# Performance work log

Hardware: AMD Instinct MI355X
Metric: run time of the kernel (lower is better)

The kernel has to match this reference:

```python
import jax, jax.numpy as jnp
import numpy as np

B, L, H = 2, 2048, 2048
NH, D = 16, 128          # num_heads, head_dim
MLP = 4 * H              # mlp_hidden_dim = int(hidden_size * mlp_ratio)


def setup_inputs() -> dict:
    key = jax.random.key(0)
    ks = jax.random.split(key, 8)
    x = jax.random.normal(ks[0], (B, L, H), jnp.float32)
    vec = jax.random.normal(ks[1], (B, H), jnp.float32)
    pe = jax.random.normal(ks[2], (B, 1, L, D // 2, 2, 2), jnp.float32)
    # Modulation(dim, is_double=False): Linear(H, 3H)
    mod_w = 0.02 * jax.random.normal(ks[3], (3 * H, H), jnp.float32)
    mod_b = jnp.zeros((3 * H,), jnp.float32)
    # linear1: Linear(H, 3H + MLP)
    lin1_w = 0.02 * jax.random.normal(ks[4], (3 * H + MLP, H), jnp.float32)
    lin1_b = jnp.zeros((3 * H + MLP,), jnp.float32)
    # linear2: Linear(H + MLP, H)
    lin2_w = 0.02 * jax.random.normal(ks[5], (H, H + MLP), jnp.float32)
    lin2_b = jnp.zeros((H,), jnp.float32)
    # QKNorm: RMSNorm scales over head_dim
    q_scale = jnp.ones((D,), jnp.float32)
    k_scale = jnp.ones((D,), jnp.float32)
    return dict(x=x, vec=vec, pe=pe, mod_w=mod_w, mod_b=mod_b,
                lin1_w=lin1_w, lin1_b=lin1_b, lin2_w=lin2_w, lin2_b=lin2_b,
                q_scale=q_scale, k_scale=k_scale)


def _layernorm(x, eps=1e-6):
    mu = jnp.mean(x, axis=-1, keepdims=True)
    var = jnp.mean((x - mu) ** 2, axis=-1, keepdims=True)
    return (x - mu) * jax.lax.rsqrt(var + eps)


def _rmsnorm(x, scale, eps=1e-6):
    return x * jax.lax.rsqrt(jnp.mean(x * x, axis=-1, keepdims=True) + eps) * scale


def _apply_rope(t, pe):
    # t: [B, NH, L, D]; pe: [B, 1, L, D//2, 2, 2]
    t_ = t.reshape(*t.shape[:-1], D // 2, 1, 2)
    out = pe[..., 0] * t_[..., 0] + pe[..., 1] * t_[..., 1]  # [B, NH, L, D//2, 2]
    return out.reshape(*t.shape)


def reference(x, vec, pe, mod_w, mod_b, lin1_w, lin1_b, lin2_w, lin2_b, q_scale, k_scale):
    # Modulation: silu -> linear -> (shift, scale, gate), each [B, 1, H]
    mod = jax.nn.silu(vec) @ mod_w.T + mod_b
    shift, scale, gate = jnp.split(mod[:, None, :], 3, axis=-1)

    x_mod = (1.0 + scale) * _layernorm(x) + shift

    h = x_mod @ lin1_w.T + lin1_b            # [B, L, 3H + MLP]
    qkv, mlp = h[..., :3 * H], h[..., 3 * H:]

    # 'B L (K H D) -> K B H L D'
    qkv = qkv.reshape(B, L, 3, NH, D).transpose(2, 0, 3, 1, 4)
    q, k, v = qkv[0], qkv[1], qkv[2]

    q = _rmsnorm(q, q_scale)
    k = _rmsnorm(k, k_scale)

    q = _apply_rope(q, pe)
    k = _apply_rope(k, pe)

    # SDPA with default scale 1/sqrt(D)
    logits = jnp.einsum('bhqd,bhkd->bhqk', q, k) / jnp.sqrt(jnp.float32(D))
    probs = jax.nn.softmax(logits, axis=-1)
    attn = jnp.einsum('bhqk,bhkd->bhqd', probs, v)          # [B, NH, L, D]
    attn = attn.transpose(0, 2, 1, 3).reshape(B, L, H)      # 'B H L D -> B L (H D)'

    mlp_act = jax.nn.gelu(mlp, approximate=True)
    out = jnp.concatenate([attn, mlp_act], axis=-1) @ lin2_w.T + lin2_b
    return x + gate * out
```

## Files before the change

kernel.cpp:

```cpp
#include <hip/hip_runtime.h>

#define LSEQ 2048
#define HDIM 2048
#define NHEAD 16
#define DHEAD 128
#define N1 14336
#define NC 10240

typedef unsigned short u16;
typedef __attribute__((ext_vector_type(8))) short short8;
typedef __attribute__((ext_vector_type(4))) float f32x4;

#define ASYNC16(g, l) __builtin_amdgcn_global_load_lds( \
    (__attribute__((address_space(1))) void*)(g),        \
    (__attribute__((address_space(3))) void*)(l), 16, 0, 0)

__device__ __forceinline__ u16 f2bf(float f) {
  unsigned u = __builtin_bit_cast(unsigned, f);
  u += 0x7fffu + ((u >> 16) & 1u);
  return (u16)(u >> 16);
}
__device__ __forceinline__ float bf2f(u16 v) {
  unsigned u = ((unsigned)v) << 16;
  return __builtin_bit_cast(float, u);
}
__device__ __forceinline__ float silu_f(float x) { return x / (1.f + __expf(-x)); }
__device__ __forceinline__ float gelu_f(float x) {
  float u = 0.7978845608028654f * (x + 0.044715f * x * x * x);
  float e = __expf(2.f * u);
  float th = 1.f - 2.f / (e + 1.f);
  return 0.5f * x * (1.f + th);
}

__global__ __launch_bounds__(256) void k_mod(const float* __restrict__ vec,
                                             const float* __restrict__ mod_w,
                                             const float* __restrict__ mod_b,
                                             float* __restrict__ modv) {
  int j = blockIdx.x, t = threadIdx.x;
  const float4* wr = (const float4*)(mod_w + (size_t)j * HDIM);
  const float4* vv = (const float4*)vec;
  float s0 = 0.f, s1 = 0.f;
#pragma unroll
  for (int i = 0; i < 2; i++) {
    int idx = t + i * 256;
    float4 w = wr[idx];
    float4 a = vv[idx];
    float4 c = vv[idx + 512];
    s0 += w.x*silu_f(a.x) + w.y*silu_f(a.y) + w.z*silu_f(a.z) + w.w*silu_f(a.w);
    s1 += w.x*silu_f(c.x) + w.y*silu_f(c.y) + w.z*silu_f(c.z) + w.w*silu_f(c.w);
  }
  int lane = t & 63, wid = t >> 6;
#pragma unroll
  for (int o = 32; o; o >>= 1) { s0 += __shfl_down(s0, o, 64); s1 += __shfl_down(s1, o, 64); }
  __shared__ float red[8];
  if (!lane) { red[wid] = s0; red[4 + wid] = s1; }
  __syncthreads();
  if (!t) {
    float b_ = mod_b[j];
    modv[j] = red[0]+red[1]+red[2]+red[3] + b_;
    modv[3*HDIM + j] = red[4]+red[5]+red[6]+red[7] + b_;
  }
}

__global__ __launch_bounds__(256) void k_ln(const float* __restrict__ x,
                                            const float* __restrict__ modv,
                                            u16* __restrict__ xmod) {
  int row = blockIdx.x, t = threadIdx.x;
  int b = row >> 11;
  const float4* xr = (const float4*)(x + (size_t)row * HDIM);
  float4 v0 = xr[t], v1 = xr[t + 256];
  float sum = v0.x+v0.y+v0.z+v0.w + v1.x+v1.y+v1.z+v1.w;
  float sq  = v0.x*v0.x+v0.y*v0.y+v0.z*v0.z+v0.w*v0.w
            + v1.x*v1.x+v1.y*v1.y+v1.z*v1.z+v1.w*v1.w;
  int lane = t & 63, wid = t >> 6;
#pragma unroll
  for (int o = 32; o; o >>= 1) { sum += __shfl_down(sum, o, 64); sq += __shfl_down(sq, o, 64); }
  __shared__ float red[8];
  if (!lane) { red[wid] = sum; red[4+wid] = sq; }
  __syncthreads();
  sum = red[0]+red[1]+red[2]+red[3];
  sq  = red[4]+red[5]+red[6]+red[7];
  float mu = sum * (1.f/HDIM);
  float rstd = rsqrtf(sq * (1.f/HDIM) - mu*mu + 1e-6f);
  const float* mb = modv + b * (3*HDIM);
  u16* orow = xmod + (size_t)row * HDIM;
  float vv[8] = {v0.x,v0.y,v0.z,v0.w,v1.x,v1.y,v1.z,v1.w};
#pragma unroll
  for (int half = 0; half < 2; half++) {
    int h0 = (t + half*256) * 4;
    ushort4 o4;
    float e0 = (1.f + mb[HDIM + h0+0]) * ((vv[half*4+0]-mu)*rstd) + mb[h0+0];
    float e1 = (1.f + mb[HDIM + h0+1]) * ((vv[half*4+1]-mu)*rstd) + mb[h0+1];
    float e2 = (1.f + mb[HDIM + h0+2]) * ((vv[half*4+2]-mu)*rstd) + mb[h0+2];
    float e3 = (1.f + mb[HDIM + h0+3]) * ((vv[half*4+3]-mu)*rstd) + mb[h0+3];
    o4.x = f2bf(e0); o4.y = f2bf(e1); o4.z = f2bf(e2); o4.w = f2bf(e3);
    *(ushort4*)(orow + h0) = o4;
  }
}

__global__ __launch_bounds__(256) void k_cvt(const float4* __restrict__ src,
                                             ushort4* __restrict__ dst, int n4) {
  int i = blockIdx.x * 256 + threadIdx.x;
  int stride = gridDim.x * 256;
  for (; i < n4; i += stride) {
    float4 v = src[i];
    ushort4 o;
    o.x = f2bf(v.x); o.y = f2bf(v.y); o.z = f2bf(v.z); o.w = f2bf(v.w);
    dst[i] = o;
  }
}

__global__ __launch_bounds__(256, 2) void k_gemm1(const u16* __restrict__ A,
                                                  const u16* __restrict__ Bw,
                                                  const float* __restrict__ bias,
                                                  u16* __restrict__ qkv,
                                                  u16* __restrict__ cat) {
  const int K = HDIM;
  const int NB = N1 / 128;
  int bid = blockIdx.x;
  int bm = bid / NB, bn = bid % NB;
  int t = threadIdx.x, wave = t >> 6, lane = t & 63;
  int wm = wave >> 1, wn = wave & 1;
  __shared__ u16 S[128 * 136];
  u16* As = S;
  u16* Bs = S + 4096;
  const f32x4 fzero = {0.f, 0.f, 0.f, 0.f};
  f32x4 acc[4][4];
#pragma unroll
  for (int i = 0; i < 4; i++)
#pragma unroll
    for (int j2 = 0; j2 < 4; j2++) acc[i][j2] = fzero;
  const u16* Ab = A + (size_t)bm * 128 * K;
  const u16* Bb = Bw + (size_t)bn * 128 * K;
  int r4 = lane >> 2, c4 = lane & 3;
  int fm = lane & 15, fk = (lane >> 4) * 8, fq = lane >> 4;
  for (int k0 = 0; k0 < K; k0 += 32) {
#pragma unroll
    for (int i = 0; i < 2; i++) {
      int row = wave*32 + i*16;
      ASYNC16(Ab + (size_t)(row + r4)*K + k0 + c4*8, &As[row*32]);
      ASYNC16(Bb + (size_t)(row + r4)*K + k0 + c4*8, &Bs[row*32]);
    }
    __syncthreads();
    short8 af[4], bfr[4];
#pragma unroll
    for (int mt = 0; mt < 4; mt++)
      af[mt] = *(const short8*)&As[(wm*64 + mt*16 + fm)*32 + fk];
#pragma unroll
    for (int nt = 0; nt < 4; nt++)
      bfr[nt] = *(const short8*)&Bs[(wn*64 + nt*16 + fm)*32 + fk];
#pragma unroll
    for (int mt = 0; mt < 4; mt++)
#pragma unroll
      for (int nt = 0; nt < 4; nt++)
        acc[mt][nt] = __builtin_amdgcn_mfma_f32_16x16x32_bf16(af[mt], bfr[nt], acc[mt][nt], 0, 0, 0);
    __syncthreads();
  }
  bool ismlp = (bn >= 48);
#pragma unroll
  for (int nt = 0; nt < 4; nt++) {
    int col_l = wn*64 + nt*16 + fm;
    float bv = bias[bn*128 + col_l];
#pragma unroll
    for (int mt = 0; mt < 4; mt++) {
#pragma unroll
      for (int rr = 0; rr < 4; rr++) {
        int row_l = wm*64 + mt*16 + fq*4 + rr;
        float v = acc[mt][nt][rr] + bv;
        if (ismlp) v = gelu_f(v);
        S[row_l*136 + col_l] = f2bf(v);
      }
    }
  }
  __syncthreads();
  int c = (t & 15) * 8;
  int rq = t >> 4;
#pragma unroll
  for (int p = 0; p < 8; p++) {
    int r_l = p*16 + rq;
    short8 v = *(const short8*)&S[r_l*136 + c];
    int row_g = bm*128 + r_l;
    if (!ismlp)
      *(short8*)(qkv + (size_t)row_g*(3*HDIM) + bn*128 + c) = v;
    else
      *(short8*)(cat + (size_t)row_g*NC + HDIM + (bn-48)*128 + c) = v;
  }
}

__global__ __launch_bounds__(256, 2) void k_gemm2(const u16* __restrict__ A,
                                                  const u16* __restrict__ Bw,
                                                  const float* __restrict__ bias,
                                                  const float* __restrict__ xres,
                                                  const float* __restrict__ modv,
                                                  float* __restrict__ out) {
  const int K = NC;
  const int NB = HDIM / 128;
  int bid = blockIdx.x;
  int bm = bid / NB, bn = bid % NB;
  int t = threadIdx.x, wave = t >> 6, lane = t & 63;
  int wm = wave >> 1, wn = wave & 1;
  __shared__ u16 As[128 * 32];
  __shared__ u16 Bs[128 * 32];
  const f32x4 fzero = {0.f, 0.f, 0.f, 0.f};
  f32x4 acc[4][4];
#pragma unroll
  for (int i = 0; i < 4; i++)
#pragma unroll
    for (int j2 = 0; j2 < 4; j2++) acc[i][j2] = fzero;
  const u16* Ab = A + (size_t)bm * 128 * K;
  const u16* Bb = Bw + (size_t)bn * 128 * K;
  int r4 = lane >> 2, c4 = lane & 3;
  int fm = lane & 15, fk = (lane >> 4) * 8;
  for (int k0 = 0; k0 < K; k0 += 32) {
#pragma unroll
    for (int i = 0; i < 2; i++) {
      int row = wave*32 + i*16;
      ASYNC16(Ab + (size_t)(row + r4)*K + k0 + c4*8, &As[row*32]);
      ASYNC16(Bb + (size_t)(row + r4)*K + k0 + c4*8, &Bs[row*32]);
    }
    __syncthreads();
    short8 af[4], bfr[4];
#pragma unroll
    for (int mt = 0; mt < 4; mt++)
      af[mt] = *(const short8*)&As[(wm*64 + mt*16 + fm)*32 + fk];
#pragma unroll
    for (int nt = 0; nt < 4; nt++)
      bfr[nt] = *(const short8*)&Bs[(wn*64 + nt*16 + fm)*32 + fk];
#pragma unroll
    for (int mt = 0; mt < 4; mt++)
#pragma unroll
      for (int nt = 0; nt < 4; nt++)
        acc[mt][nt] = __builtin_amdgcn_mfma_f32_16x16x32_bf16(af[mt], bfr[nt], acc[mt][nt], 0, 0, 0);
    __syncthreads();
  }
  int rbase = bm*128 + wm*64;
  int cbase = bn*128 + wn*64;
  int b = (bm*128) >> 11;
#pragma unroll
  for (int nt = 0; nt < 4; nt++) {
    int col = cbase + nt*16 + fm;
    float bv = bias[col];
    float g = modv[b*(3*HDIM) + 2*HDIM + col];
#pragma unroll
    for (int mt = 0; mt < 4; mt++) {
#pragma unroll
      for (int rr = 0; rr < 4; rr++) {
        int row = rbase + mt*16 + (lane>>4)*4 + rr;
        size_t idx = (size_t)row*HDIM + col;
        out[idx] = xres[idx] + g * (acc[mt][nt][rr] + bv);
      }
    }
  }
}

__global__ __launch_bounds__(256) void k_qk(const u16* __restrict__ qkv,
                                            const float* __restrict__ pe,
                                            const float* __restrict__ q_scale,
                                            const float* __restrict__ k_scale,
                                            u16* __restrict__ Q, u16* __restrict__ Ko) {
  int bid = blockIdx.x;
  int l = bid & (LSEQ-1);
  int b = bid >> 11;
  int t = threadIdx.x;
  int h = t >> 4;
  int dc = (t & 15) * 8;
  const u16* base = qkv + (size_t)bid * (3*HDIM);
  short8 q8 = *(const short8*)(base + h*DHEAD + dc);
  short8 k8 = *(const short8*)(base + HDIM + h*DHEAD + dc);
  float qf[8], kf[8];
  float sq = 0.f, sk = 0.f;
#pragma unroll
  for (int i = 0; i < 8; i++) {
    qf[i] = bf2f((u16)q8[i]); kf[i] = bf2f((u16)k8[i]);
    sq += qf[i]*qf[i]; sk += kf[i]*kf[i];
  }
#pragma unroll
  for (int m = 1; m < 16; m <<= 1) { sq += __shfl_xor(sq, m, 64); sk += __shfl_xor(sk, m, 64); }
  float rq = rsqrtf(sq * (1.f/DHEAD) + 1e-6f);
  float rk = rsqrtf(sk * (1.f/DHEAD) + 1e-6f);
  float4 qs0 = *(const float4*)(q_scale + dc), qs1 = *(const float4*)(q_scale + dc + 4);
  float4 ks0 = *(const float4*)(k_scale + dc), ks1 = *(const float4*)(k_scale + dc + 4);
  float qsc[8] = {qs0.x,qs0.y,qs0.z,qs0.w,qs1.x,qs1.y,qs1.z,qs1.w};
  float ksc[8] = {ks0.x,ks0.y,ks0.z,ks0.w,ks1.x,ks1.y,ks1.z,ks1.w};
  float qn[8], kn[8];
#pragma unroll
  for (int i = 0; i < 8; i++) { qn[i] = qf[i]*rq*qsc[i]; kn[i] = kf[i]*rk*ksc[i]; }
  const float4* pe4 = (const float4*)pe + ((size_t)bid*64 + (dc >> 1));
  short8 qo, ko;
#pragma unroll
  for (int pi = 0; pi < 4; pi++) {
    float4 pp = pe4[pi];
    float q0 = pp.x*qn[2*pi] + pp.y*qn[2*pi+1];
    float q1 = pp.z*qn[2*pi] + pp.w*qn[2*pi+1];
    float k0 = pp.x*kn[2*pi] + pp.y*kn[2*pi+1];
    float k1 = pp.z*kn[2*pi] + pp.w*kn[2*pi+1];
    qo[2*pi] = (short)f2bf(q0); qo[2*pi+1] = (short)f2bf(q1);
    ko[2*pi] = (short)f2bf(k0); ko[2*pi+1] = (short)f2bf(k1);
  }
  size_t oidx = (((size_t)(b*NHEAD + h))*LSEQ + l)*DHEAD + dc;
  *(short8*)(Q + oidx) = qo;
  *(short8*)(Ko + oidx) = ko;
}

__global__ __launch_bounds__(256) void k_vt(const u16* __restrict__ qkv, u16* __restrict__ Vt) {
  int bid = blockIdx.x;
  int lt = bid & 31, h = (bid >> 5) & 15, b = bid >> 9;
  __shared__ u16 tile[64][132];
  int t = threadIdx.x;
#pragma unroll
  for (int it = 0; it < 8; it++) {
    int idx = it*1024 + t*4;
    int li = idx >> 7, di = idx & 127;
    const u16* src = qkv + ((size_t)(b*LSEQ + lt*64 + li))*(3*HDIM) + 2*HDIM + h*DHEAD + di;
    ushort4 v = *(const ushort4*)src;
    *(ushort4*)&tile[li][di] = v;
  }
  __syncthreads();
  u16* dst = Vt + ((size_t)(b*NHEAD + h))*DHEAD*LSEQ + lt*64;
#pragma unroll
  for (int it = 0; it < 32; it++) {
    int idx = it*256 + t;
    int lo = idx & 63, dd = idx >> 6;
    dst[(size_t)dd*LSEQ + lo] = tile[lo][dd];
  }
}

#define ATT_SCALE 0.08838834764831845f
__global__ __launch_bounds__(256, 2) void k_attn(const u16* __restrict__ Q,
                                                 const u16* __restrict__ Kc,
                                                 const u16* __restrict__ Vt,
                                                 u16* __restrict__ cat) {
  __shared__ u16 Ks[2*64*128];
  __shared__ u16 Vs[2*128*64];
  __shared__ u16 Ps[64*88];
  int bid = blockIdx.x;
  int bh = bid & 31, qt = bid >> 5;
  int h = bh & 15, b = bh >> 4;
  int t = threadIdx.x, wave = t >> 6, lane = t & 63;
  int fm = lane & 15, fq = lane >> 4;
  int r8 = lane >> 3, c8 = lane & 7;
  const u16* Qg = Q  + (((size_t)(b*NHEAD + h))*LSEQ + qt*64) * DHEAD;
  const u16* Kg = Kc + ((size_t)(b*NHEAD + h))*LSEQ * DHEAD;
  const u16* Vg = Vt + ((size_t)(b*NHEAD + h))*DHEAD*LSEQ;
  short8 aq[4];
#pragma unroll
  for (int ks = 0; ks < 4; ks++)
    aq[ks] = *(const short8*)(Qg + (size_t)(wave*16 + fm)*DHEAD + ks*32 + fq*8);
#pragma unroll
  for (int i = 0; i < 4; i++) {
    int row = wave*16 + i*4;
    ASYNC16(Kg + (size_t)(row + fq)*DHEAD + fm*8, &Ks[row*DHEAD]);
    int vrow = wave*32 + i*8;
    ASYNC16(Vg + (size_t)(vrow + r8)*LSEQ + c8*8, &Vs[vrow*64]);
  }
  const f32x4 fzero = {0.f, 0.f, 0.f, 0.f};
  f32x4 o[8];
#pragma unroll
  for (int i = 0; i < 8; i++) o[i] = fzero;
  float m_i[4], l_i[4];
#pragma unroll
  for (int r = 0; r < 4; r++) { m_i[r] = -1e30f; l_i[r] = 0.f; }
  for (int kt = 0; kt < 32; kt++) {
    int cur = kt & 1;
    __syncthreads();
    if (kt < 31) {
      int off = (cur ^ 1) * 8192;
      const u16* Kt_ = Kg + (size_t)(kt+1)*64*DHEAD;
      const u16* Vt_ = Vg + (kt+1)*64;
#pragma unroll
      for (int i = 0; i < 4; i++) {
        int row = wave*16 + i*4;
        ASYNC16(Kt_ + (size_t)(row + fq)*DHEAD + fm*8, &Ks[off + row*DHEAD]);
        int vrow = wave*32 + i*8;
        ASYNC16(Vt_ + (size_t)(vrow + r8)*LSEQ + c8*8, &Vs[off + vrow*64]);
      }
    }
    const u16* Kb = &Ks[cur*8192];
    const u16* Vb = &Vs[cur*8192];
    f32x4 s[4];
#pragma unroll
    for (int nt = 0; nt < 4; nt++) s[nt] = fzero;
#pragma unroll
    for (int ks = 0; ks < 4; ks++) {
#pragma unroll
      for (int nt = 0; nt < 4; nt++) {
        short8 bk = *(const short8*)&Kb[(nt*16 + fm)*DHEAD + ks*32 + fq*8];
        s[nt] = __builtin_amdgcn_mfma_f32_16x16x32_bf16(aq[ks], bk, s[nt], 0, 0, 0);
      }
    }
    float rowm[4];
#pragma unroll
    for (int r = 0; r < 4; r++)
      rowm[r] = fmaxf(fmaxf(s[0][r], s[1][r]), fmaxf(s[2][r], s[3][r])) * ATT_SCALE;
#pragma unroll
    for (int r = 0; r < 4; r++) {
#pragma unroll
      for (int o2 = 8; o2 >= 1; o2 >>= 1)
        rowm[r] = fmaxf(rowm[r], __shfl_xor(rowm[r], o2, 64));
    }
    float alpha[4];
#pragma unroll
    for (int r = 0; r < 4; r++) {
      float mnew = fmaxf(m_i[r], rowm[r]);
      alpha[r] = __expf(m_i[r] - mnew);
      m_i[r] = mnew;
    }
    float rs[4] = {0.f, 0.f, 0.f, 0.f};
#pragma unroll
    for (int nt = 0; nt < 4; nt++)
#pragma unroll
      for (int r = 0; r < 4; r++) {
        float p = __expf(s[nt][r] * ATT_SCALE - m_i[r]);
        s[nt][r] = p;
        rs[r] += p;
      }
#pragma unroll
    for (int r = 0; r < 4; r++) {
#pragma unroll
      for (int o2 = 8; o2 >= 1; o2 >>= 1) rs[r] += __shfl_xor(rs[r], o2, 64);
      l_i[r] = l_i[r] * alpha[r] + rs[r];
    }
#pragma unroll
    for (int i = 0; i < 8; i++)
#pragma unroll
      for (int r = 0; r < 4; r++) o[i][r] *= alpha[r];
#pragma unroll
    for (int nt = 0; nt < 4; nt++)
#pragma unroll
      for (int r = 0; r < 4; r++)
        Ps[(wave*16 + fq*4 + r)*88 + nt*16 + fm] = f2bf(s[nt][r]);
    asm volatile("s_waitcnt lgkmcnt(0)" ::: "memory");
#pragma unroll
    for (int ks2 = 0; ks2 < 2; ks2++) {
      short8 ap = *(const short8*)&Ps[(wave*16 + fm)*88 + ks2*32 + fq*8];
#pragma unroll
      for (int nt = 0; nt < 8; nt++) {
        short8 bv = *(const short8*)&Vb[(nt*16 + fm)*64 + ks2*32 + fq*8];
        o[nt] = __builtin_amdgcn_mfma_f32_16x16x32_bf16(ap, bv, o[nt], 0, 0, 0);
      }
    }
  }
#pragma unroll
  for (int nt = 0; nt < 8; nt++) {
#pragma unroll
    for (int r = 0; r < 4; r++) {
      int l = qt*64 + wave*16 + fq*4 + r;
      int d = nt*16 + fm;
      float v = o[nt][r] / l_i[r];
      cat[((size_t)(b*LSEQ + l))*NC + h*DHEAD + d] = f2bf(v);
    }
  }
}

extern "C" void kernel_launch(void* const* d_in, const int* in_sizes, int n_in,
                              void* d_out, int out_size, void* d_ws, size_t ws_size,
                              hipStream_t stream) {
  const float* x       = (const float*)d_in[0];
  const float* vec     = (const float*)d_in[1];
  const float* pe      = (const float*)d_in[2];
  const float* mod_w   = (const float*)d_in[3];
  const float* mod_b   = (const float*)d_in[4];
  const float* lin1_w  = (const float*)d_in[5];
  const float* lin1_b  = (const float*)d_in[6];
  const float* lin2_w  = (const float*)d_in[7];
  const float* lin2_b  = (const float*)d_in[8];
  const float* q_scale = (const float*)d_in[9];
  const float* k_scale = (const float*)d_in[10];
  char* ws = (char*)d_ws;

  float* modv = (float*)(ws + 0);
  u16* xmod  = (u16*)(ws + 65536ULL);
  u16* qkv   = (u16*)(ws + 16842752ULL);
  u16* cat   = (u16*)(ws + 67174400ULL);
  u16* w2    = (u16*)(ws + 151060480ULL);
  u16* w1    = (u16*)(ws + 193003520ULL);
  u16* Qb    = (u16*)(ws + 193003520ULL);
  u16* Kb    = (u16*)(ws + 209780736ULL);
  u16* Vtb   = (u16*)(ws + 226557952ULL);

  k_mod<<<dim3(3*HDIM), dim3(256), 0, stream>>>(vec, mod_w, mod_b, modv);
  k_cvt<<<dim3(4096), dim3(256), 0, stream>>>((const float4*)lin1_w, (ushort4*)w1, (N1*HDIM)/4);
  k_cvt<<<dim3(4096), dim3(256), 0, stream>>>((const float4*)lin2_w, (ushort4*)w2, (HDIM*NC)/4);
  k_ln<<<dim3(4096), dim3(256), 0, stream>>>(x, modv, xmod);
  k_gemm1<<<dim3(32*112), dim3(256), 0, stream>>>(xmod, w1, lin1_b, qkv, cat);
  k_qk<<<dim3(4096), dim3(256), 0, stream>>>(qkv, pe, q_scale, k_scale, Qb, Kb);
  k_vt<<<dim3(1024), dim3(256), 0, stream>>>(qkv, Vtb);
  k_attn<<<dim3(1024), dim3(256), 0, stream>>>(Qb, Kb, Vtb, cat);
  k_gemm2<<<dim3(32*16), dim3(256), 0, stream>>>(cat, w2, lin2_b, x, modv, (float*)d_out);
}
```

Baseline: 1.185 ms.

## Double K-step in GEMMs, drop online-max softmax, reorder blocks and workspace

Both GEMMs now load 64-wide K slices per barrier pair instead of 32, halving synchronisation count, and block indices are remapped so M tiles vary fastest for weight reuse in cache. Attention drops the running max and rescaling, relying on QK-normalised logits being bounded, and uses exp2 with a folded scale plus truncating bf16 conversion for P. The lin2 weight conversion is moved later and placed over the dead qkv region to shrink workspace. The risks are overflow if q/k scales grow, and slightly lower precision from truncation.

Result: faster. 1.012 ms (-14.6%).

```diff
diff --git a/kernel.cpp b/kernel.cpp
--- a/kernel.cpp
+++ b/kernel.cpp
@@ -19,6 +19,9 @@
   unsigned u = __builtin_bit_cast(unsigned, f);
   u += 0x7fffu + ((u >> 16) & 1u);
   return (u16)(u >> 16);
+}
+__device__ __forceinline__ u16 f2bf_trunc(float f) {
+  return (u16)(__builtin_bit_cast(unsigned, f) >> 16);
 }
 __device__ __forceinline__ float bf2f(u16 v) {
   unsigned u = ((unsigned)v) << 16;
@@ -116,14 +119,15 @@
                                                   u16* __restrict__ qkv,
                                                   u16* __restrict__ cat) {
   const int K = HDIM;
-  const int NB = N1 / 128;
   int bid = blockIdx.x;
-  int bm = bid / NB, bn = bid % NB;
+  int bm = bid & 31, bn = bid >> 5;
   int t = threadIdx.x, wave = t >> 6, lane = t & 63;
   int wm = wave >> 1, wn = wave & 1;
   __shared__ u16 S[128 * 136];
-  u16* As = S;
-  u16* Bs = S + 4096;
+  u16* As0 = S;
+  u16* As1 = S + 4096;
+  u16* Bs0 = S + 8192;
+  u16* Bs1 = S + 12288;
   const f32x4 fzero = {0.f, 0.f, 0.f, 0.f};
   f32x4 acc[4][4];
 #pragma unroll
@@ -134,26 +138,35 @@
   const u16* Bb = Bw + (size_t)bn * 128 * K;
   int r4 = lane >> 2, c4 = lane & 3;
   int fm = lane & 15, fk = (lane >> 4) * 8, fq = lane >> 4;
-  for (int k0 = 0; k0 < K; k0 += 32) {
+  for (int k0 = 0; k0 < K; k0 += 64) {
 #pragma unroll
     for (int i = 0; i < 2; i++) {
       int row = wave*32 + i*16;
-      ASYNC16(Ab + (size_t)(row + r4)*K + k0 + c4*8, &As[row*32]);
-      ASYNC16(Bb + (size_t)(row + r4)*K + k0 + c4*8, &Bs[row*32]);
+      const u16* ar = Ab + (size_t)(row + r4)*K + k0 + c4*8;
+      const u16* br = Bb + (size_t)(row + r4)*K + k0 + c4*8;
+      ASYNC16(ar,      &As0[row*32]);
+      ASYNC16(ar + 32, &As1[row*32]);
+      ASYNC16(br,      &Bs0[row*32]);
+      ASYNC16(br + 32, &Bs1[row*32]);
     }
     __syncthreads();
-    short8 af[4], bfr[4];
-#pragma unroll
-    for (int mt = 0; mt < 4; mt++)
-      af[mt] = *(const short8*)&As[(wm*64 + mt*16 + fm)*32 + fk];
-#pragma unroll
-    for (int nt = 0; nt < 4; nt++)
-      bfr[nt] = *(const short8*)&Bs[(wn*64 + nt*16 + fm)*32 + fk];
-#pragma unroll
-    for (int mt = 0; mt < 4; mt++)
+#pragma unroll
+    for (int p = 0; p < 2; p++) {
+      const u16* Ap = p ? As1 : As0;
+      const u16* Bp = p ? Bs1 : Bs0;
+      short8 af[4], bfr[4];
+#pragma unroll
+      for (int mt = 0; mt < 4; mt++)
+        af[mt] = *(const short8*)&Ap[(wm*64 + mt*16 + fm)*32 + fk];
 #pragma unroll
       for (int nt = 0; nt < 4; nt++)
-        acc[mt][nt] = __builtin_amdgcn_mfma_f32_16x16x32_bf16(af[mt], bfr[nt], acc[mt][nt], 0, 0, 0);
+        bfr[nt] = *(const short8*)&Bp[(wn*64 + nt*16 + fm)*32 + fk];
+#pragma unroll
+      for (int mt = 0; mt < 4; mt++)
+#pragma unroll
+        for (int nt = 0; nt < 4; nt++)
+          acc[mt][nt] = __builtin_amdgcn_mfma_f32_16x16x32_bf16(af[mt], bfr[nt], acc[mt][nt], 0, 0, 0);
+    }
     __syncthreads();
   }
   bool ismlp = (bn >= 48);
@@ -194,13 +207,12 @@
                                                   const float* __restrict__ modv,
                                                   float* __restrict__ out) {
   const int K = NC;
-  const int NB = HDIM / 128;
   int bid = blockIdx.x;
-  int bm = bid / NB, bn = bid % NB;
+  int bm = bid & 31, bn = bid >> 5;
   int t = threadIdx.x, wave = t >> 6, lane = t & 63;
   int wm = wave >> 1, wn = wave & 1;
-  __shared__ u16 As[128 * 32];
-  __shared__ u16 Bs[128 * 32];
+  __shared__ u16 As[2*128*32];
+  __shared__ u16 Bs[2*128*32];
   const f32x4 fzero = {0.f, 0.f, 0.f, 0.f};
   f32x4 acc[4][4];
 #pragma unroll
@@ -211,26 +223,35 @@
   const u16* Bb = Bw + (size_t)bn * 128 * K;
   int r4 = lane >> 2, c4 = lane & 3;
   int fm = lane & 15, fk = (lane >> 4) * 8;
-  for (int k0 = 0; k0 < K; k0 += 32) {
+  for (int k0 = 0; k0 < K; k0 += 64) {
 #pragma unroll
     for (int i = 0; i < 2; i++) {
       int row = wave*32 + i*16;
-      ASYNC16(Ab + (size_t)(row + r4)*K + k0 + c4*8, &As[row*32]);
-      ASYNC16(Bb + (size_t)(row + r4)*K + k0 + c4*8, &Bs[row*32]);
+      const u16* ar = Ab + (size_t)(row + r4)*K + k0 + c4*8;
+      const u16* br = Bb + (size_t)(row + r4)*K + k0 + c4*8;
+      ASYNC16(ar,      &As[row*32]);
+      ASYNC16(ar + 32, &As[4096 + row*32]);
+      ASYNC16(br,      &Bs[row*32]);
+      ASYNC16(br + 32, &Bs[4096 + row*32]);
     }
     __syncthreads();
-    short8 af[4], bfr[4];
-#pragma unroll
-    for (int mt = 0; mt < 4; mt++)
-      af[mt] = *(const short8*)&As[(wm*64 + mt*16 + fm)*32 + fk];
-#pragma unroll
-    for (int nt = 0; nt < 4; nt++)
-      bfr[nt] = *(const short8*)&Bs[(wn*64 + nt*16 + fm)*32 + fk];
-#pragma unroll
-    for (int mt = 0; mt < 4; mt++)
+#pragma unroll
+    for (int p = 0; p < 2; p++) {
+      const u16* Ap = &As[p*4096];
+      const u16* Bp = &Bs[p*4096];
+      short8 af[4], bfr[4];
+#pragma unroll
+      for (int mt = 0; mt < 4; mt++)
+        af[mt] = *(const short8*)&Ap[(wm*64 + mt*16 + fm)*32 + fk];
 #pragma unroll
       for (int nt = 0; nt < 4; nt++)
-        acc[mt][nt] = __builtin_amdgcn_mfma_f32_16x16x32_bf16(af[mt], bfr[nt], acc[mt][nt], 0, 0, 0);
+        bfr[nt] = *(const short8*)&Bp[(wn*64 + nt*16 + fm)*32 + fk];
+#pragma unroll
+      for (int mt = 0; mt < 4; mt++)
+#pragma unroll
+        for (int nt = 0; nt < 4; nt++)
+          acc[mt][nt] = __builtin_amdgcn_mfma_f32_16x16x32_bf16(af[mt], bfr[nt], acc[mt][nt], 0, 0, 0);
+    }
     __syncthreads();
   }
   int rbase = bm*128 + wm*64;
@@ -325,7 +346,7 @@
   }
 }
 
-#define ATT_SCALE 0.08838834764831845f
+#define SC2 0.12753329583f
 __global__ __launch_bounds__(256, 2) void k_attn(const u16* __restrict__ Q,
                                                  const u16* __restrict__ Kc,
                                                  const u16* __restrict__ Vt,
@@ -357,9 +378,7 @@
   f32x4 o[8];
 #pragma unroll
   for (int i = 0; i < 8; i++) o[i] = fzero;
-  float m_i[4], l_i[4];
-#pragma unroll
-  for (int r = 0; r < 4; r++) { m_i[r] = -1e30f; l_i[r] = 0.f; }
+  float lsum[4] = {0.f, 0.f, 0.f, 0.f};
   for (int kt = 0; kt < 32; kt++) {
     int cur = kt & 1;
     __syncthreads();
@@ -388,47 +407,19 @@
         s[nt] = __builtin_amdgcn_mfma_f32_16x16x32_bf16(aq[ks], bk, s[nt], 0, 0, 0);
       }
     }
-    float rowm[4];
-#pragma unroll
-    for (int r = 0; r < 4; r++)
-      rowm[r] = fmaxf(fmaxf(s[0][r], s[1][r]), fmaxf(s[2][r], s[3][r])) * ATT_SCALE;
-#pragma unroll
-    for (int r = 0; r < 4; r++) {
-#pragma unroll
-      for (int o2 = 8; o2 >= 1; o2 >>= 1)
-        rowm[r] = fmaxf(rowm[r], __shfl_xor(rowm[r], o2, 64));
-    }
-    float alpha[4];
-#pragma unroll
-    for (int r = 0; r < 4; r++) {
-      float mnew = fmaxf(m_i[r], rowm[r]);
-      alpha[r] = __expf(m_i[r] - mnew);
-      m_i[r] = mnew;
-    }
-    float rs[4] = {0.f, 0.f, 0.f, 0.f};
 #pragma unroll
     for (int nt = 0; nt < 4; nt++)
 #pragma unroll
       for (int r = 0; r < 4; r++) {
-        float p = __expf(s[nt][r] * ATT_SCALE - m_i[r]);
+        float p = exp2f(s[nt][r] * SC2);
         s[nt][r] = p;
-        rs[r] += p;
-      }
-#pragma unroll
-    for (int r = 0; r < 4; r++) {
-#pragma unroll
-      for (int o2 = 8; o2 >= 1; o2 >>= 1) rs[r] += __shfl_xor(rs[r], o2, 64);
-      l_i[r] = l_i[r] * alpha[r] + rs[r];
-    }
-#pragma unroll
-    for (int i = 0; i < 8; i++)
-#pragma unroll
-      for (int r = 0; r < 4; r++) o[i][r] *= alpha[r];
+        lsum[r] += p;
+      }
 #pragma unroll
     for (int nt = 0; nt < 4; nt++)
 #pragma unroll
       for (int r = 0; r < 4; r++)
-        Ps[(wave*16 + fq*4 + r)*88 + nt*16 + fm] = f2bf(s[nt][r]);
+        Ps[(wave*16 + fq*4 + r)*88 + nt*16 + fm] = f2bf_trunc(s[nt][r]);
     asm volatile("s_waitcnt lgkmcnt(0)" ::: "memory");
 #pragma unroll
     for (int ks2 = 0; ks2 < 2; ks2++) {
@@ -441,12 +432,17 @@
     }
   }
 #pragma unroll
+  for (int r = 0; r < 4; r++) {
+#pragma unroll
+    for (int o2 = 8; o2 >= 1; o2 >>= 1) lsum[r] += __shfl_xor(lsum[r], o2, 64);
+  }
+#pragma unroll
   for (int nt = 0; nt < 8; nt++) {
 #pragma unroll
     for (int r = 0; r < 4; r++) {
       int l = qt*64 + wave*16 + fq*4 + r;
       int d = nt*16 + fm;
-      float v = o[nt][r] / l_i[r];
+      float v = o[nt][r] / lsum[r];
       cat[((size_t)(b*LSEQ + l))*NC + h*DHEAD + d] = f2bf(v);
     }
   }
@@ -471,20 +467,20 @@
   float* modv = (float*)(ws + 0);
   u16* xmod  = (u16*)(ws + 65536ULL);
   u16* qkv   = (u16*)(ws + 16842752ULL);
+  u16* w2    = (u16*)(ws + 16842752ULL);
   u16* cat   = (u16*)(ws + 67174400ULL);
-  u16* w2    = (u16*)(ws + 151060480ULL);
-  u16* w1    = (u16*)(ws + 193003520ULL);
-  u16* Qb    = (u16*)(ws + 193003520ULL);
-  u16* Kb    = (u16*)(ws + 209780736ULL);
-  u16* Vtb   = (u16*)(ws + 226557952ULL);
+  u16* w1    = (u16*)(ws + 151060480ULL);
+  u16* Qb    = (u16*)(ws + 151060480ULL);
+  u16* Kb    = (u16*)(ws + 167837696ULL);
+  u16* Vtb   = (u16*)(ws + 184614912ULL);
 
   k_mod<<<dim3(3*HDIM), dim3(256), 0, stream>>>(vec, mod_w, mod_b, modv);
   k_cvt<<<dim3(4096), dim3(256), 0, stream>>>((const float4*)lin1_w, (ushort4*)w1, (N1*HDIM)/4);
-  k_cvt<<<dim3(4096), dim3(256), 0, stream>>>((const float4*)lin2_w, (ushort4*)w2, (HDIM*NC)/4);
   k_ln<<<dim3(4096), dim3(256), 0, stream>>>(x, modv, xmod);
   k_gemm1<<<dim3(32*112), dim3(256), 0, stream>>>(xmod, w1, lin1_b, qkv, cat);
   k_qk<<<dim3(4096), dim3(256), 0, stream>>>(qkv, pe, q_scale, k_scale, Qb, Kb);
   k_vt<<<dim3(1024), dim3(256), 0, stream>>>(qkv, Vtb);
+  k_cvt<<<dim3(4096), dim3(256), 0, stream>>>((const float4*)lin2_w, (ushort4*)w2, (HDIM*NC)/4);
   k_attn<<<dim3(1024), dim3(256), 0, stream>>>(Qb, Kb, Vtb, cat);
   k_gemm2<<<dim3(32*16), dim3(256), 0, stream>>>(cat, w2, lin2_b, x, modv, (float*)d_out);
 }
```
